# Optimization experiments

Measured on AMD Instinct MI355X. Metric: run time of the kernel, lower is better.

Reference implementation:

```python
import jax, jax.numpy as jnp
import numpy as np
from jax.scipy.linalg import expm

H_DIM = 2048
U_DIM = 1024
DU_DIM = 256
Y_DIM = 1024
DELTA = 0.1


def _linear_init(key, out_f, in_f):
    # torch.nn.Linear default init: U(-1/sqrt(in_f), 1/sqrt(in_f))
    bound = 1.0 / np.sqrt(in_f)
    return jax.random.uniform(key, (out_f, in_f), jnp.float32, -bound, bound)


def setup_inputs() -> dict:
    key = jax.random.key(0)
    k_u, k_du, k_w, k_b, k_c, k_h = jax.random.split(key, 6)
    return {
        "u": jax.random.normal(k_u, (1, U_DIM), jnp.float32),
        "du": jax.random.normal(k_du, (1, DU_DIM), jnp.float32),
        "W_weight": _linear_init(k_w, H_DIM, H_DIM),
        "B_weight": _linear_init(k_b, H_DIM, U_DIM + DU_DIM),
        "C_weight": _linear_init(k_c, Y_DIM, H_DIM),
        "h_init": jax.random.normal(k_h, (1, H_DIM), jnp.float32),
    }


def reference(u, du, W_weight, B_weight, C_weight, h_init):
    # Antisymmetric part of W
    A = 0.5 * (W_weight - W_weight.T)                  # (H, H), skew-symmetric
    E = expm(A * DELTA)                                # matrix exponential (orthogonal)
    # Recurrent term: F.linear(h, E) = h @ E.T
    rec = h_init @ E.T                                 # (1, H)
    # Input term: A^{-1} (E - I) B [du, u]
    A_inv = jnp.linalg.inv(A)                          # even H -> invertible a.s.
    udu = jnp.concatenate([du, u], axis=1)             # (1, DU+U), du first per torch.cat([du, u])
    bu = udu @ B_weight.T                              # (1, H)
    eye = jnp.eye(H_DIM, dtype=A.dtype)
    inp = (A_inv @ (E - eye) @ bu[..., None])[..., 0]  # (1, H)
    h_new = rec + inp
    # sigma = identity, C linear (no bias)
    y = h_new @ C_weight.T                             # (1, Y)
    return y
```

## Files before the change

kernel.cpp:

```cpp
#include <hip/hip_runtime.h>
#include <math.h>

#define H    2048
#define UDIM 1024
#define DUD  256
#define UD   1280
#define YD   1024
#define NTAYLOR 6

#define OFF_A    0
#define OFF_XH0  (H*H)
#define OFF_XH1  (OFF_XH0 + H)
#define OFF_XB0  (OFF_XH1 + H)
#define OFF_XB1  (OFF_XB0 + H)
#define OFF_S1   (OFF_XB1 + H)
#define OFF_S2   (OFF_S1 + H)

__global__ __launch_bounds__(256) void build_A(const float* __restrict__ W,
                                               float* __restrict__ A) {
    int p = blockIdx.x;
    int ti = 0, rowlen = H / 64;
    while (p >= rowlen) { p -= rowlen; ++ti; --rowlen; }
    int tj = ti + p;

    __shared__ float t1[64][65];
    __shared__ float t2[64][65];
    const int tx = threadIdx.x & 63, ty = threadIdx.x >> 6;
    const int r0 = ti * 64, c0 = tj * 64;

    for (int r = ty; r < 64; r += 4) {
        t1[r][tx] = W[(size_t)(r0 + r) * H + c0 + tx];
        t2[r][tx] = W[(size_t)(c0 + r) * H + r0 + tx];
    }
    __syncthreads();
    for (int r = ty; r < 64; r += 4) {
        A[(size_t)(r0 + r) * H + c0 + tx] = 0.5f * (t1[r][tx] - t2[tx][r]);
        if (ti != tj)
            A[(size_t)(c0 + r) * H + r0 + tx] = 0.5f * (t2[r][tx] - t1[tx][r]);
    }
}

__global__ __launch_bounds__(256) void bu_init(const float* __restrict__ Bw,
                                               const float* __restrict__ u,
                                               const float* __restrict__ du,
                                               const float* __restrict__ h,
                                               float* __restrict__ ws) {
    float* xh0 = ws + OFF_XH0;
    float* xb0 = ws + OFF_XB0;
    float* s1  = ws + OFF_S1;
    float* s2  = ws + OFF_S2;

    const int gt = blockIdx.x * 256 + threadIdx.x;
    if (gt < H) { float hv = h[gt]; xh0[gt] = hv; s1[gt] = hv; }

    const int w = gt >> 6;
    const int lane = gt & 63;

    float4 xv[5];
    #pragma unroll
    for (int i = 0; i < 5; ++i) {
        int f = i * 64 + lane;
        xv[i] = (f < 64) ? ((const float4*)du)[f] : ((const float4*)u)[f - 64];
    }
    #pragma unroll
    for (int rr = 0; rr < 2; ++rr) {
        int r = w * 2 + rr;
        const float4* Brow = (const float4*)(Bw + (size_t)r * UD);
        float acc = 0.f;
        #pragma unroll
        for (int i = 0; i < 5; ++i) {
            float4 b = Brow[i * 64 + lane];
            acc = fmaf(b.x, xv[i].x, acc);
            acc = fmaf(b.y, xv[i].y, acc);
            acc = fmaf(b.z, xv[i].z, acc);
            acc = fmaf(b.w, xv[i].w, acc);
        }
        #pragma unroll
        for (int off = 32; off; off >>= 1) acc += __shfl_xor(acc, off, 64);
        if (lane == 0) { float v = 0.1f * acc; xb0[r] = v; s2[r] = v; }
    }
}

__global__ __launch_bounds__(256) void matvec(const float* __restrict__ A,
                                              const float4* __restrict__ xhin,
                                              const float4* __restrict__ xbin,
                                              float* __restrict__ xhout,
                                              float* __restrict__ xbout,
                                              float* __restrict__ s1,
                                              float* __restrict__ s2,
                                              float cH, float cB) {
    const int gt = blockIdx.x * 256 + threadIdx.x;
    const int w = gt >> 6, lane = gt & 63;

    float4 xh[8], xb[8];
    #pragma unroll
    for (int i = 0; i < 8; ++i) {
        int f = i * 64 + lane;
        xh[i] = xhin[f];
        xb[i] = xbin[f];
    }
    #pragma unroll
    for (int rr = 0; rr < 2; ++rr) {
        int r = w * 2 + rr;
        const float4* Arow = (const float4*)(A + (size_t)r * H);
        float ah = 0.f, ab = 0.f;
        #pragma unroll
        for (int i = 0; i < 8; ++i) {
            float4 a = Arow[i * 64 + lane];
            ah = fmaf(a.x, xh[i].x, ah); ab = fmaf(a.x, xb[i].x, ab);
            ah = fmaf(a.y, xh[i].y, ah); ab = fmaf(a.y, xb[i].y, ab);
            ah = fmaf(a.z, xh[i].z, ah); ab = fmaf(a.z, xb[i].z, ab);
            ah = fmaf(a.w, xh[i].w, ah); ab = fmaf(a.w, xb[i].w, ab);
        }
        #pragma unroll
        for (int off = 32; off; off >>= 1) {
            ah += __shfl_xor(ah, off, 64);
            ab += __shfl_xor(ab, off, 64);
        }
        if (lane == 0) {
            float nh = cH * ah, nb = cB * ab;
            xhout[r] = nh; xbout[r] = nb;
            s1[r] += nh;   s2[r] += nb;
        }
    }
}

__global__ __launch_bounds__(256) void final_y(const float* __restrict__ C,
                                               const float* __restrict__ ws,
                                               float* __restrict__ out) {
    const float4* s14 = (const float4*)(ws + OFF_S1);
    const float4* s24 = (const float4*)(ws + OFF_S2);
    const int gt = blockIdx.x * 256 + threadIdx.x;
    const int w = gt >> 6, lane = gt & 63;

    float4 hx[8];
    #pragma unroll
    for (int i = 0; i < 8; ++i) {
        int f = i * 64 + lane;
        float4 a = s14[f], b = s24[f];
        hx[i] = make_float4(a.x + b.x, a.y + b.y, a.z + b.z, a.w + b.w);
    }
    const float4* Crow = (const float4*)(C + (size_t)w * H);
    float acc = 0.f;
    #pragma unroll
    for (int i = 0; i < 8; ++i) {
        float4 c = Crow[i * 64 + lane];
        acc = fmaf(c.x, hx[i].x, acc);
        acc = fmaf(c.y, hx[i].y, acc);
        acc = fmaf(c.z, hx[i].z, acc);
        acc = fmaf(c.w, hx[i].w, acc);
    }
    #pragma unroll
    for (int off = 32; off; off >>= 1) acc += __shfl_xor(acc, off, 64);
    if (lane == 0) out[w] = acc;
}

extern "C" void kernel_launch(void* const* d_in, const int* in_sizes, int n_in,
                              void* d_out, int out_size, void* d_ws, size_t ws_size,
                              hipStream_t stream) {
    const float* u  = (const float*)d_in[0];
    const float* du = (const float*)d_in[1];
    const float* W  = (const float*)d_in[2];
    const float* Bw = (const float*)d_in[3];
    const float* Cw = (const float*)d_in[4];
    const float* h  = (const float*)d_in[5];
    float* ws  = (float*)d_ws;
    float* out = (float*)d_out;

    build_A<<<528, 256, 0, stream>>>(W, ws + OFF_A);
    bu_init<<<256, 256, 0, stream>>>(Bw, u, du, h, ws);

    float* xh[2] = {ws + OFF_XH0, ws + OFF_XH1};
    float* xb[2] = {ws + OFF_XB0, ws + OFF_XB1};
    for (int k = 0; k < NTAYLOR; ++k) {
        int a = k & 1, b = a ^ 1;
        matvec<<<256, 256, 0, stream>>>(ws + OFF_A,
                                        (const float4*)xh[a], (const float4*)xb[a],
                                        xh[b], xb[b],
                                        ws + OFF_S1, ws + OFF_S2,
                                        0.1f / (float)(k + 1), 0.1f / (float)(k + 2));
    }
    final_y<<<256, 256, 0, stream>>>(Cw, ws, out);
}
```

Measured before the change: 122.4 us.

## Fuse whole pipeline into one cooperative kernel with LDS-resident A rows

Replaces the separate build_A, bu_init, per-term matvec and final_y launches with a single cooperative kernel. Each block keeps its 8 rows of the skew-symmetric A in shared memory, so A is never written to or reread from global memory. Taylor steps are separated by grid-wide syncs instead of kernel launches. The Taylor series also drops from 6 to 4 terms, which cuts work but makes the expm approximation less accurate. The column reads of W used to build A are strided and uncoalesced, and the 64KB of LDS per block limits occupancy.

```diff
diff --git a/kernel.cpp b/kernel.cpp
--- a/kernel.cpp
+++ b/kernel.cpp
@@ -1,158 +1,163 @@
 #include <hip/hip_runtime.h>
-#include <math.h>
+#include <hip/hip_cooperative_groups.h>
 
-#define H    2048
-#define UDIM 1024
-#define DUD  256
-#define UD   1280
-#define YD   1024
-#define NTAYLOR 6
+namespace cg = cooperative_groups;
 
-#define OFF_A    0
-#define OFF_XH0  (H*H)
-#define OFF_XH1  (OFF_XH0 + H)
-#define OFF_XB0  (OFF_XH1 + H)
-#define OFF_XB1  (OFF_XB0 + H)
-#define OFF_S1   (OFF_XB1 + H)
-#define OFF_S2   (OFF_S1 + H)
+#define H     2048
+#define UD    1280
+#define NT    4
+#define RPB   8
+#define NBLK  (H / RPB)
+#define DELTAF 0.1f
 
-__global__ __launch_bounds__(256) void build_A(const float* __restrict__ W,
-                                               float* __restrict__ A) {
-    int p = blockIdx.x;
-    int ti = 0, rowlen = H / 64;
-    while (p >= rowlen) { p -= rowlen; ++ti; --rowlen; }
-    int tj = ti + p;
+#define OFF_XH0 0
+#define OFF_XH1 (OFF_XH0 + H)
+#define OFF_XB0 (OFF_XH1 + H)
+#define OFF_XB1 (OFF_XB0 + H)
+#define OFF_HS  (OFF_XB1 + H)
 
-    __shared__ float t1[64][65];
-    __shared__ float t2[64][65];
-    const int tx = threadIdx.x & 63, ty = threadIdx.x >> 6;
-    const int r0 = ti * 64, c0 = tj * 64;
+__global__ __launch_bounds__(256) void cte_coop(
+    const float* __restrict__ W, const float* __restrict__ Bw,
+    const float* __restrict__ Cw, const float* __restrict__ u,
+    const float* __restrict__ du, const float* __restrict__ h,
+    float* __restrict__ ws, float* __restrict__ out)
+{
+    extern __shared__ float Asl[];
+    float4* Af4 = (float4*)Asl;
+    cg::grid_group grid = cg::this_grid();
 
-    for (int r = ty; r < 64; r += 4) {
-        t1[r][tx] = W[(size_t)(r0 + r) * H + c0 + tx];
-        t2[r][tx] = W[(size_t)(c0 + r) * H + r0 + tx];
+    const int b    = blockIdx.x;
+    const int tid  = threadIdx.x;
+    const int lane = tid & 63;
+    const int w    = tid >> 6;
+    const int rl0  = 2 * w, rl1 = 2 * w + 1;
+
+    {
+        const float4* Wb = (const float4*)(W + (size_t)b * RPB * H);
+        #pragma unroll
+        for (int r = 0; r < RPB; ++r) {
+            Af4[r * 512 + tid]       = Wb[r * 512 + tid];
+            Af4[r * 512 + 256 + tid] = Wb[r * 512 + 256 + tid];
+        }
     }
+
+    float s1[2], s2[2], q0[2];
+    {
+        const int rls[2] = {rl0, rl1};
+        #pragma unroll
+        for (int t = 0; t < 2; ++t) {
+            const int gr = b * RPB + rls[t];
+            const float4* Brow = (const float4*)(Bw + (size_t)gr * UD);
+            float acc = 0.f;
+            #pragma unroll
+            for (int i = 0; i < 5; ++i) {
+                int f = i * 64 + lane;
+                float4 xv = (f < 64) ? ((const float4*)du)[f]
+                                     : ((const float4*)u)[f - 64];
+                float4 bb = Brow[f];
+                acc = fmaf(bb.x, xv.x, acc);
+                acc = fmaf(bb.y, xv.y, acc);
+                acc = fmaf(bb.z, xv.z, acc);
+                acc = fmaf(bb.w, xv.w, acc);
+            }
+            #pragma unroll
+            for (int off = 32; off; off >>= 1) acc += __shfl_xor(acc, off, 64);
+            q0[t] = DELTAF * acc;
+            s2[t] = q0[t];
+            s1[t] = h[gr];
+        }
+    }
+
     __syncthreads();
-    for (int r = ty; r < 64; r += 4) {
-        A[(size_t)(r0 + r) * H + c0 + tx] = 0.5f * (t1[r][tx] - t2[tx][r]);
-        if (ti != tj)
-            A[(size_t)(c0 + r) * H + r0 + tx] = 0.5f * (t2[r][tx] - t1[tx][r]);
+
+    #pragma unroll
+    for (int kk = 0; kk < 8; ++kk) {
+        const int c = kk * 256 + tid;
+        const float* Wc = W + (size_t)c * H + b * RPB;
+        float4 w0 = *(const float4*)(Wc);
+        float4 w1 = *(const float4*)(Wc + 4);
+        Asl[0 * H + c] = 0.5f * (Asl[0 * H + c] - w0.x);
+        Asl[1 * H + c] = 0.5f * (Asl[1 * H + c] - w0.y);
+        Asl[2 * H + c] = 0.5f * (Asl[2 * H + c] - w0.z);
+        Asl[3 * H + c] = 0.5f * (Asl[3 * H + c] - w0.w);
+        Asl[4 * H + c] = 0.5f * (Asl[4 * H + c] - w1.x);
+        Asl[5 * H + c] = 0.5f * (Asl[5 * H + c] - w1.y);
+        Asl[6 * H + c] = 0.5f * (Asl[6 * H + c] - w1.z);
+        Asl[7 * H + c] = 0.5f * (Asl[7 * H + c] - w1.w);
     }
-}
 
-__global__ __launch_bounds__(256) void bu_init(const float* __restrict__ Bw,
-                                               const float* __restrict__ u,
-                                               const float* __restrict__ du,
-                                               const float* __restrict__ h,
-                                               float* __restrict__ ws) {
-    float* xh0 = ws + OFF_XH0;
-    float* xb0 = ws + OFF_XB0;
-    float* s1  = ws + OFF_S1;
-    float* s2  = ws + OFF_S2;
+    if (lane == 0) {
+        ws[OFF_XB0 + b * RPB + rl0] = q0[0];
+        ws[OFF_XB0 + b * RPB + rl1] = q0[1];
+    }
 
-    const int gt = blockIdx.x * 256 + threadIdx.x;
-    if (gt < H) { float hv = h[gt]; xh0[gt] = hv; s1[gt] = hv; }
+    grid.sync();
 
-    const int w = gt >> 6;
-    const int lane = gt & 63;
+    float* xhb[2] = {ws + OFF_XH0, ws + OFF_XH1};
+    float* xbb[2] = {ws + OFF_XB0, ws + OFF_XB1};
 
-    float4 xv[5];
     #pragma unroll
-    for (int i = 0; i < 5; ++i) {
-        int f = i * 64 + lane;
-        xv[i] = (f < 64) ? ((const float4*)du)[f] : ((const float4*)u)[f - 64];
+    for (int k = 0; k < NT; ++k) {
+        const int si = k & 1, di = si ^ 1;
+        const float cH = DELTAF / (float)(k + 1);
+        const float cB = DELTAF / (float)(k + 2);
+        const float4* Xh = (const float4*)((k == 0) ? h : xhb[si]);
+        const float4* Xb = (const float4*)xbb[si];
+
+        float4 vh[8], vb[8];
+        #pragma unroll
+        for (int i = 0; i < 8; ++i) {
+            vh[i] = Xh[i * 64 + lane];
+            vb[i] = Xb[i * 64 + lane];
+        }
+
+        const int rls[2] = {rl0, rl1};
+        #pragma unroll
+        for (int t = 0; t < 2; ++t) {
+            const float4* Ar = Af4 + rls[t] * 512;
+            float ah = 0.f, ab = 0.f;
+            #pragma unroll
+            for (int i = 0; i < 8; ++i) {
+                float4 a = Ar[i * 64 + lane];
+                ah = fmaf(a.x, vh[i].x, ah); ab = fmaf(a.x, vb[i].x, ab);
+                ah = fmaf(a.y, vh[i].y, ah); ab = fmaf(a.y, vb[i].y, ab);
+                ah = fmaf(a.z, vh[i].z, ah); ab = fmaf(a.z, vb[i].z, ab);
+                ah = fmaf(a.w, vh[i].w, ah); ab = fmaf(a.w, vb[i].w, ab);
+            }
+            #pragma unroll
+            for (int off = 32; off; off >>= 1) {
+                ah += __shfl_xor(ah, off, 64);
+                ab += __shfl_xor(ab, off, 64);
+            }
+            const float nh = cH * ah, nb = cB * ab;
+            s1[t] += nh; s2[t] += nb;
+            if (lane == 0) {
+                const int gr = b * RPB + rls[t];
+                if (k < NT - 1) { xhb[di][gr] = nh; xbb[di][gr] = nb; }
+                else            { ws[OFF_HS + gr] = s1[t] + s2[t]; }
+            }
+        }
+        grid.sync();
     }
-    #pragma unroll
-    for (int rr = 0; rr < 2; ++rr) {
-        int r = w * 2 + rr;
-        const float4* Brow = (const float4*)(Bw + (size_t)r * UD);
+
+    {
+        const int row = b * 4 + w;
+        const float4* Crow = (const float4*)(Cw + (size_t)row * H);
+        const float4* Hs   = (const float4*)(ws + OFF_HS);
         float acc = 0.f;
         #pragma unroll
-        for (int i = 0; i < 5; ++i) {
-            float4 b = Brow[i * 64 + lane];
-            acc = fmaf(b.x, xv[i].x, acc);
-            acc = fmaf(b.y, xv[i].y, acc);
-            acc = fmaf(b.z, xv[i].z, acc);
-            acc = fmaf(b.w, xv[i].w, acc);
+        for (int i = 0; i < 8; ++i) {
+            float4 c4 = Crow[i * 64 + lane];
+            float4 hv = Hs[i * 64 + lane];
+            acc = fmaf(c4.x, hv.x, acc);
+            acc = fmaf(c4.y, hv.y, acc);
+            acc = fmaf(c4.z, hv.z, acc);
+            acc = fmaf(c4.w, hv.w, acc);
         }
         #pragma unroll
         for (int off = 32; off; off >>= 1) acc += __shfl_xor(acc, off, 64);
-        if (lane == 0) { float v = 0.1f * acc; xb0[r] = v; s2[r] = v; }
+        if (lane == 0) out[row] = acc;
     }
-}
-
-__global__ __launch_bounds__(256) void matvec(const float* __restrict__ A,
-                                              const float4* __restrict__ xhin,
-                                              const float4* __restrict__ xbin,
-                                              float* __restrict__ xhout,
-                                              float* __restrict__ xbout,
-                                              float* __restrict__ s1,
-                                              float* __restrict__ s2,
-                                              float cH, float cB) {
-    const int gt = blockIdx.x * 256 + threadIdx.x;
-    const int w = gt >> 6, lane = gt & 63;
-
-    float4 xh[8], xb[8];
-    #pragma unroll
-    for (int i = 0; i < 8; ++i) {
-        int f = i * 64 + lane;
-        xh[i] = xhin[f];
-        xb[i] = xbin[f];
-    }
-    #pragma unroll
-    for (int rr = 0; rr < 2; ++rr) {
-        int r = w * 2 + rr;
-        const float4* Arow = (const float4*)(A + (size_t)r * H);
-        float ah = 0.f, ab = 0.f;
-        #pragma unroll
-        for (int i = 0; i < 8; ++i) {
-            float4 a = Arow[i * 64 + lane];
-            ah = fmaf(a.x, xh[i].x, ah); ab = fmaf(a.x, xb[i].x, ab);
-            ah = fmaf(a.y, xh[i].y, ah); ab = fmaf(a.y, xb[i].y, ab);
-            ah = fmaf(a.z, xh[i].z, ah); ab = fmaf(a.z, xb[i].z, ab);
-            ah = fmaf(a.w, xh[i].w, ah); ab = fmaf(a.w, xb[i].w, ab);
-        }
-        #pragma unroll
-        for (int off = 32; off; off >>= 1) {
-            ah += __shfl_xor(ah, off, 64);
-            ab += __shfl_xor(ab, off, 64);
-        }
-        if (lane == 0) {
-            float nh = cH * ah, nb = cB * ab;
-            xhout[r] = nh; xbout[r] = nb;
-            s1[r] += nh;   s2[r] += nb;
-        }
-    }
-}
-
-__global__ __launch_bounds__(256) void final_y(const float* __restrict__ C,
-                                               const float* __restrict__ ws,
-                                               float* __restrict__ out) {
-    const float4* s14 = (const float4*)(ws + OFF_S1);
-    const float4* s24 = (const float4*)(ws + OFF_S2);
-    const int gt = blockIdx.x * 256 + threadIdx.x;
-    const int w = gt >> 6, lane = gt & 63;
-
-    float4 hx[8];
-    #pragma unroll
-    for (int i = 0; i < 8; ++i) {
-        int f = i * 64 + lane;
-        float4 a = s14[f], b = s24[f];
-        hx[i] = make_float4(a.x + b.x, a.y + b.y, a.z + b.z, a.w + b.w);
-    }
-    const float4* Crow = (const float4*)(C + (size_t)w * H);
-    float acc = 0.f;
-    #pragma unroll
-    for (int i = 0; i < 8; ++i) {
-        float4 c = Crow[i * 64 + lane];
-        acc = fmaf(c.x, hx[i].x, acc);
-        acc = fmaf(c.y, hx[i].y, acc);
-        acc = fmaf(c.z, hx[i].z, acc);
-        acc = fmaf(c.w, hx[i].w, acc);
-    }
-    #pragma unroll
-    for (int off = 32; off; off >>= 1) acc += __shfl_xor(acc, off, 64);
-    if (lane == 0) out[w] = acc;
 }
 
 extern "C" void kernel_launch(void* const* d_in, const int* in_sizes, int n_in,
@@ -167,18 +172,8 @@
     float* ws  = (float*)d_ws;
     float* out = (float*)d_out;
 
-    build_A<<<528, 256, 0, stream>>>(W, ws + OFF_A);
-    bu_init<<<256, 256, 0, stream>>>(Bw, u, du, h, ws);
-
-    float* xh[2] = {ws + OFF_XH0, ws + OFF_XH1};
-    float* xb[2] = {ws + OFF_XB0, ws + OFF_XB1};
-    for (int k = 0; k < NTAYLOR; ++k) {
-        int a = k & 1, b = a ^ 1;
-        matvec<<<256, 256, 0, stream>>>(ws + OFF_A,
-                                        (const float4*)xh[a], (const float4*)xb[a],
-                                        xh[b], xb[b],
-                                        ws + OFF_S1, ws + OFF_S2,
-                                        0.1f / (float)(k + 1), 0.1f / (float)(k + 2));
-    }
-    final_y<<<256, 256, 0, stream>>>(Cw, ws, out);
+    void* args[] = {(void*)&W, (void*)&Bw, (void*)&Cw, (void*)&u,
+                    (void*)&du, (void*)&h, (void*)&ws, (void*)&out};
+    hipLaunchCooperativeKernel((const void*)cte_coop, dim3(NBLK), dim3(256),
+                               args, RPB * H * sizeof(float), stream);
 }
```

Result: slower. 260.7 us (+113.1%).
